# Kernel tuning notes

Measured on AMD Instinct MI355X. Metric: run time of the kernel, lower is better.

## Reference

```python
import jax, jax.numpy as jnp
import numpy as np

N, E, G = 30000, 240000, 1500
EMB, NODE_DIM, EDGE_DIM, TASKS = 300, 9, 3, 12
L_ENC, L_RAT = 5, 2
GAMMA, T_CON = 0.4, 0.2


def _w(key, shape, fan_in):
    return jax.random.normal(key, shape, jnp.float32) / np.float32(np.sqrt(fan_in))


def setup_inputs() -> dict:
    key = jax.random.key(0)
    ks = jax.random.split(key, 32)
    inp = {}
    inp['x'] = jax.random.normal(ks[0], (N, NODE_DIM), jnp.float32)
    inp['edge_attr'] = jax.random.normal(ks[1], (E, EDGE_DIM), jnp.float32)
    inp['edge_index'] = jax.random.randint(ks[2], (2, E), 0, N, jnp.int32)
    b = jnp.sort(jax.random.randint(ks[3], (N,), 0, G, jnp.int32))
    inp['batch'] = b.at[0].set(0).at[-1].set(G - 1)
    u = jax.random.uniform(ks[4], (N, 2), jnp.float32, 1e-6, 1.0 - 1e-6)
    inp['gumbel'] = -jnp.log(-jnp.log(u))  # standard Gumbel noise (tau=1)
    inp['perm'] = jax.random.permutation(ks[5], G).astype(jnp.int32)
    inp['W_enc'] = _w(ks[6], (NODE_DIM, EMB), NODE_DIM)
    inp['b_enc'] = jnp.zeros((EMB,), jnp.float32)
    inp['We_g'] = _w(ks[7], (L_ENC, EDGE_DIM, EMB), EDGE_DIM)
    inp['be_g'] = jnp.zeros((L_ENC, EMB), jnp.float32)
    inp['W1_g'] = _w(ks[8], (L_ENC, EMB, 2 * EMB), EMB)
    inp['b1_g'] = jnp.zeros((L_ENC, 2 * EMB), jnp.float32)
    inp['W2_g'] = _w(ks[9], (L_ENC, 2 * EMB, EMB), 2 * EMB)
    inp['b2_g'] = jnp.zeros((L_ENC, EMB), jnp.float32)
    inp['We_r'] = _w(ks[10], (L_RAT, EDGE_DIM, EMB), EDGE_DIM)
    inp['be_r'] = jnp.zeros((L_RAT, EMB), jnp.float32)
    inp['W1_r'] = _w(ks[11], (L_RAT, EMB, 2 * EMB), EMB)
    inp['b1_r'] = jnp.zeros((L_RAT, 2 * EMB), jnp.float32)
    inp['W2_r'] = _w(ks[12], (L_RAT, 2 * EMB, EMB), 2 * EMB)
    inp['b2_r'] = jnp.zeros((L_RAT, EMB), jnp.float32)
    inp['Wg1'] = _w(ks[13], (EMB, 2 * EMB), EMB)
    inp['bg1'] = jnp.zeros((2 * EMB,), jnp.float32)
    inp['Wg2'] = _w(ks[14], (2 * EMB, 2), 2 * EMB)
    inp['bg2'] = jnp.zeros((2,), jnp.float32)
    inp['Wp1'] = _w(ks[15], (EMB, 2 * EMB), EMB)
    inp['bp1'] = jnp.zeros((2 * EMB,), jnp.float32)
    inp['Wp2'] = _w(ks[16], (2 * EMB, TASKS), 2 * EMB)
    inp['bp2'] = jnp.zeros((TASKS,), jnp.float32)
    return inp


def _gin_stack(x, src, dst, edge_attr, We, be, W1, b1, W2, b2):
    # GIN-style message passing with edge features, residual, JK='last'.
    L = We.shape[0]
    for l in range(L):
        e = edge_attr @ We[l] + be[l]                               # [E, EMB]
        msg = jax.nn.relu(x[src] + e)                                # gather [E, EMB]
        agg = jax.ops.segment_sum(msg, dst, num_segments=x.shape[0])  # scatter [N, EMB]
        h = jax.nn.relu((agg + x) @ W1[l] + b1[l]) @ W2[l] + b2[l]
        if l < L - 1:
            h = jax.nn.relu(h)
        x = x + h  # residual
    return x


def _mlp2(h, Wa, ba, Wb, bb):
    # Linear -> (BN=identity in eval) -> ReLU -> (Dropout=identity) -> Linear
    return jax.nn.relu(h @ Wa + ba) @ Wb + bb


def _forward(x, edge_attr, gumbel, W_enc, b_enc, We_g, be_g, W1_g, b1_g, W2_g, b2_g,
             We_r, be_r, W1_r, b1_r, W2_r, b2_r, Wg1, bg1, Wg2, bg2, Wp1, bp1, Wp2, bp2,
             edge_index, batch, perm):
    src, dst = edge_index[0], edge_index[1]
    cnt = jnp.clip(jax.ops.segment_sum(jnp.ones((x.shape[0],), jnp.float32), batch, num_segments=G), 1.0)[:, None]

    def gmean(v):
        return jax.ops.segment_sum(v, batch, num_segments=G) / cnt

    x_feat = x @ W_enc + b_enc                                      # node encoder
    h_node = _gin_stack(x_feat, src, dst, edge_attr, We_g, be_g, W1_g, b1_g, W2_g, b2_g)
    x_rat = _gin_stack(x_feat, src, dst, edge_attr, We_r, be_r, W1_r, b1_r, W2_r, b2_r)

    gate_logits = _mlp2(x_rat, Wg1, bg1, Wg2, bg2)                  # [N, 2]
    gate = jax.nn.softmax(gate_logits + gumbel, axis=-1)[:, 1:2]     # gumbel-softmax (soft), keep last col

    h_r = gmean(gate * h_node)
    h_env = gmean((1.0 - gate) * h_node)
    r_num = jax.ops.segment_sum(gate, batch, num_segments=G) + 1e-8
    env_num = jax.ops.segment_sum(1.0 - gate, batch, num_segments=G) + 1e-8

    pred_rem = _mlp2(h_r, Wp1, bp1, Wp2, bp2)
    loss_reg = jnp.abs(r_num / (r_num + env_num) - GAMMA).mean()

    h_out = gmean(h_node)
    na = jnp.linalg.norm(h_r, axis=1)
    nb = jnp.linalg.norm(h_out, axis=1)
    nc = jnp.linalg.norm(h_env, axis=1)
    sim = jnp.exp((h_r @ h_out.T) / (na[:, None] * nb[None, :] + 1e-8) / T_CON)
    sim_cp = jnp.exp((h_r @ h_env.T) / (na[:, None] * nc[None, :] + 1e-8) / T_CON)
    pos = jnp.diagonal(sim)
    loss_con = -jnp.log(pos / (sim_cp.sum(axis=1) + pos)).mean()

    pred_rep = _mlp2(h_r + h_env[perm], Wp1, bp1, Wp2, bp2)
    return pred_rep, pred_rem, loss_reg, loss_con


def reference(x, edge_attr, gumbel, W_enc, b_enc, We_g, be_g, W1_g, b1_g, W2_g, b2_g,
              We_r, be_r, W1_r, b1_r, W2_r, b2_r, Wg1, bg1, Wg2, bg2, Wp1, bp1, Wp2, bp2,
              edge_index, batch, perm):
    return _forward(x, edge_attr, gumbel, W_enc, b_enc, We_g, be_g, W1_g, b1_g, W2_g, b2_g,
                    We_r, be_r, W1_r, b1_r, W2_r, b2_r, Wg1, bg1, Wg2, bg2, Wp1, bp1, Wp2, bp2,
                    edge_index, batch, perm)
```

## Files before the change

### kernel.cpp

```cpp
#include <hip/hip_runtime.h>
#include <hip/hip_bf16.h>

typedef __hip_bfloat16 bf16;
typedef __attribute__((ext_vector_type(8))) short bf16x8;
typedef __attribute__((ext_vector_type(4))) float f32x4;

#define NN 30000
#define NE 240000
#define NG 1500
#define EMB 300
#define HID 600
#define NTASK 12
#define SEM 320
#define SHID 608
#define CG 75
#define NBLK_SCAN 118

__device__ __forceinline__ float tof(bf16 v){ return __bfloat162float(v); }
__device__ __forceinline__ bf16  tob(float v){ return __float2bfloat16(v); }
__device__ __forceinline__ float b2f(unsigned short u){ return __uint_as_float(((unsigned)u)<<16); }

__global__ __launch_bounds__(256) void k_zero_i(int* __restrict__ p, int n){
    int i = blockIdx.x*256 + threadIdx.x;
    if (i < n) p[i] = 0;
}

__global__ __launch_bounds__(256) void k_hist(const int* __restrict__ dst, int* __restrict__ deg){
    int e = blockIdx.x*256 + threadIdx.x;
    if (e < NE) atomicAdd(&deg[dst[e]], 1);
}

__global__ __launch_bounds__(256) void k_scanA(const int* __restrict__ deg, int* __restrict__ bsum){
    __shared__ int red[256];
    int b = blockIdx.x, t = threadIdx.x;
    int i = b*256 + t;
    red[t] = (i < NN) ? deg[i] : 0;
    __syncthreads();
    for (int off=128; off>0; off>>=1){ if (t<off) red[t]+=red[t+off]; __syncthreads(); }
    if (t==0) bsum[b] = red[0];
}

__global__ __launch_bounds__(128) void k_scanB(const int* __restrict__ bsum, int* __restrict__ boff){
    __shared__ int s[128];
    int t = threadIdx.x;
    int v = (t < NBLK_SCAN) ? bsum[t] : 0;
    s[t] = v;
    __syncthreads();
    for (int off=1; off<128; off<<=1){
        int add = (t>=off) ? s[t-off] : 0;
        __syncthreads();
        s[t] += add;
        __syncthreads();
    }
    if (t < NBLK_SCAN) boff[t] = s[t] - v;
}

__global__ __launch_bounds__(256) void k_scanC(const int* __restrict__ deg, const int* __restrict__ boff,
                                               int* __restrict__ indptr, int* __restrict__ cursor){
    __shared__ int s[256];
    int b = blockIdx.x, t = threadIdx.x;
    int i = b*256 + t;
    int v = (i < NN) ? deg[i] : 0;
    s[t] = v;
    __syncthreads();
    for (int off=1; off<256; off<<=1){
        int add = (t>=off) ? s[t-off] : 0;
        __syncthreads();
        s[t] += add;
        __syncthreads();
    }
    int excl = s[t] - v + boff[b];
    if (i < NN){ indptr[i] = excl; cursor[i] = excl; }
    if (i == 0) indptr[NN] = NE;
}

__global__ __launch_bounds__(256) void k_scatter(const int* __restrict__ dst, int* __restrict__ cursor,
                                                 int* __restrict__ eid){
    int e = blockIdx.x*256 + threadIdx.x;
    if (e < NE){ int p = atomicAdd(&cursor[dst[e]], 1); eid[p] = e; }
}

__global__ __launch_bounds__(256) void k_eprep(const int* __restrict__ eid, const int* __restrict__ src,
                                               const float* __restrict__ eattr, float4* __restrict__ epack){
    int k = blockIdx.x*256 + threadIdx.x;
    if (k >= NE) return;
    int e = eid[k];
    float4 p;
    p.x = __int_as_float(src[e]);
    p.y = eattr[e*3]; p.z = eattr[e*3+1]; p.w = eattr[e*3+2];
    epack[k] = p;
}

__global__ __launch_bounds__(256) void k_gstart(const int* __restrict__ batch, int* __restrict__ gstart){
    int g = blockIdx.x*256 + threadIdx.x;
    if (g > NG) return;
    if (g == NG){ gstart[NG] = NN; return; }
    int lo=0, hi=NN;
    while (lo<hi){ int mid=(lo+hi)>>1; if (batch[mid] < g) lo=mid+1; else hi=mid; }
    gstart[g] = lo;
}

__global__ __launch_bounds__(256) void k_wprep(const float* __restrict__ W, bf16* __restrict__ Wt,
                                               int K, int Kp, int N){
    __shared__ float t[32][33];
    const float* Wz = W + (size_t)blockIdx.z*K*N;
    bf16* Wtz = Wt + (size_t)blockIdx.z*N*Kp;
    int n0 = blockIdx.x*32, k0 = blockIdx.y*32;
    int tx = threadIdx.x & 31, ty = threadIdx.x >> 5;
    #pragma unroll
    for (int i=0;i<4;i++){
        int k = k0 + ty + i*8, n = n0 + tx;
        t[ty+i*8][tx] = (k<K && n<N) ? Wz[(size_t)k*N+n] : 0.f;
    }
    __syncthreads();
    #pragma unroll
    for (int i=0;i<4;i++){
        int n = n0 + ty + i*8, k = k0 + tx;
        if (n<N && k<Kp) Wtz[(size_t)n*Kp+k] = tob(t[tx][ty+i*8]);
    }
}

__global__ __launch_bounds__(256) void k_encoder(const float* __restrict__ x, const float* __restrict__ W,
                                                 const float* __restrict__ b, bf16* __restrict__ xfeat){
    int idx = blockIdx.x*256 + threadIdx.x;
    if (idx >= NN*EMB) return;
    int n = idx / EMB, c = idx - n*EMB;
    float acc = b[c];
    #pragma unroll
    for (int k=0;k<9;k++) acc += x[n*9+k] * W[k*EMB+c];
    xfeat[(size_t)n*SEM + c] = tob(acc);
}

__global__ __launch_bounds__(256) void k_agg4(const bf16* __restrict__ cur, const float* __restrict__ We,
                      const float* __restrict__ be, const float4* __restrict__ epack,
                      const int* __restrict__ indptr, bf16* __restrict__ apx){
    int idx = blockIdx.x*256 + threadIdx.x;
    if (idx >= NN*CG) return;
    int n = idx / CG, cg = idx - n*CG;
    int c0 = cg*4;
    float w0[4], w1[4], w2[4], bbv[4], acc[4];
    #pragma unroll
    for (int j=0;j<4;j++){
        w0[j] = We[c0+j]; w1[j] = We[EMB+c0+j]; w2[j] = We[2*EMB+c0+j]; bbv[j] = be[c0+j];
    }
    ushort4 hs = *(const ushort4*)&cur[(size_t)n*SEM + c0];
    acc[0]=b2f(hs.x); acc[1]=b2f(hs.y); acc[2]=b2f(hs.z); acc[3]=b2f(hs.w);
    int k  = indptr[n], k1 = indptr[n+1];

    auto accum4 = [&](float4 e0, float4 e1, float4 e2, float4 e3,
                      ushort4 ha, ushort4 hb, ushort4 hc, ushort4 hd){
        float fa[4] = {b2f(ha.x), b2f(ha.y), b2f(ha.z), b2f(ha.w)};
        float fb[4] = {b2f(hb.x), b2f(hb.y), b2f(hb.z), b2f(hb.w)};
        float fc[4] = {b2f(hc.x), b2f(hc.y), b2f(hc.z), b2f(hc.w)};
        float fd[4] = {b2f(hd.x), b2f(hd.y), b2f(hd.z), b2f(hd.w)};
        #pragma unroll
        for (int j=0;j<4;j++){
            float va = fa[j] + e0.y*w0[j] + e0.z*w1[j] + e0.w*w2[j] + bbv[j];
            float vb = fb[j] + e1.y*w0[j] + e1.z*w1[j] + e1.w*w2[j] + bbv[j];
            float vc = fc[j] + e2.y*w0[j] + e2.z*w1[j] + e2.w*w2[j] + bbv[j];
            float vd = fd[j] + e3.y*w0[j] + e3.z*w1[j] + e3.w*w2[j] + bbv[j];
            acc[j] += fmaxf(va, 0.f) + fmaxf(vb, 0.f) + fmaxf(vc, 0.f) + fmaxf(vd, 0.f);
        }
    };

    if (k + 4 <= k1){
        float4 e0 = epack[k], e1 = epack[k+1], e2 = epack[k+2], e3 = epack[k+3];
        ushort4 h0 = *(const ushort4*)&cur[(size_t)__float_as_int(e0.x)*SEM + c0];
        ushort4 h1 = *(const ushort4*)&cur[(size_t)__float_as_int(e1.x)*SEM + c0];
        ushort4 h2 = *(const ushort4*)&cur[(size_t)__float_as_int(e2.x)*SEM + c0];
        ushort4 h3 = *(const ushort4*)&cur[(size_t)__float_as_int(e3.x)*SEM + c0];
        while (k + 8 <= k1){
            float4 f0 = epack[k+4], f1 = epack[k+5], f2 = epack[k+6], f3 = epack[k+7];
            ushort4 g0 = *(const ushort4*)&cur[(size_t)__float_as_int(f0.x)*SEM + c0];
            ushort4 g1 = *(const ushort4*)&cur[(size_t)__float_as_int(f1.x)*SEM + c0];
            ushort4 g2 = *(const ushort4*)&cur[(size_t)__float_as_int(f2.x)*SEM + c0];
            ushort4 g3 = *(const ushort4*)&cur[(size_t)__float_as_int(f3.x)*SEM + c0];
            accum4(e0,e1,e2,e3, h0,h1,h2,h3);
            e0=f0; e1=f1; e2=f2; e3=f3;
            h0=g0; h1=g1; h2=g2; h3=g3;
            k += 4;
        }
        accum4(e0,e1,e2,e3, h0,h1,h2,h3);
        k += 4;
    }
    for (; k < k1; k++){
        float4 e0 = epack[k];
        int s0 = __float_as_int(e0.x);
        ushort4 ha = *(const ushort4*)&cur[(size_t)s0*SEM + c0];
        float fa[4] = {b2f(ha.x), b2f(ha.y), b2f(ha.z), b2f(ha.w)};
        #pragma unroll
        for (int j=0;j<4;j++){
            float va = fa[j] + e0.y*w0[j] + e0.z*w1[j] + e0.w*w2[j] + bbv[j];
            acc[j] += fmaxf(va, 0.f);
        }
    }
    ushort4 o;
    o.x = __bfloat16_as_ushort(tob(acc[0]));
    o.y = __bfloat16_as_ushort(tob(acc[1]));
    o.z = __bfloat16_as_ushort(tob(acc[2]));
    o.w = __bfloat16_as_ushort(tob(acc[3]));
    *(ushort4*)&apx[(size_t)n*SEM + c0] = o;
}

__global__ __launch_bounds__(256) void k_agg4d(const bf16* __restrict__ cur,
                      const float* __restrict__ WeA, const float* __restrict__ beA,
                      const float* __restrict__ WeB, const float* __restrict__ beB,
                      const float4* __restrict__ epack, const int* __restrict__ indptr,
                      bf16* __restrict__ apxA, bf16* __restrict__ apxB){
    int idx = blockIdx.x*256 + threadIdx.x;
    if (idx >= NN*CG) return;
    int n = idx / CG, cg = idx - n*CG;
    int c0 = cg*4;
    float a0[4], a1[4], a2[4], ab[4], accA[4];
    float b0[4], b1[4], b2[4], bb[4], accB[4];
    #pragma unroll
    for (int j=0;j<4;j++){
        a0[j]=WeA[c0+j]; a1[j]=WeA[EMB+c0+j]; a2[j]=WeA[2*EMB+c0+j]; ab[j]=beA[c0+j];
        b0[j]=WeB[c0+j]; b1[j]=WeB[EMB+c0+j]; b2[j]=WeB[2*EMB+c0+j]; bb[j]=beB[c0+j];
    }
    ushort4 hs = *(const ushort4*)&cur[(size_t)n*SEM + c0];
    float fs[4] = {b2f(hs.x), b2f(hs.y), b2f(hs.z), b2f(hs.w)};
    #pragma unroll
    for (int j=0;j<4;j++){ accA[j]=fs[j]; accB[j]=fs[j]; }
    int k = indptr[n], k1 = indptr[n+1];
    for (; k+2 <= k1; k += 2){
        float4 e0 = epack[k], e1 = epack[k+1];
        int s0 = __float_as_int(e0.x), s1 = __float_as_int(e1.x);
        ushort4 ha = *(const ushort4*)&cur[(size_t)s0*SEM + c0];
        ushort4 hb = *(const ushort4*)&cur[(size_t)s1*SEM + c0];
        float fa[4] = {b2f(ha.x), b2f(ha.y), b2f(ha.z), b2f(ha.w)};
        float fb[4] = {b2f(hb.x), b2f(hb.y), b2f(hb.z), b2f(hb.w)};
        #pragma unroll
        for (int j=0;j<4;j++){
            accA[j] += fmaxf(fa[j] + e0.y*a0[j] + e0.z*a1[j] + e0.w*a2[j] + ab[j], 0.f)
                     + fmaxf(fb[j] + e1.y*a0[j] + e1.z*a1[j] + e1.w*a2[j] + ab[j], 0.f);
            accB[j] += fmaxf(fa[j] + e0.y*b0[j] + e0.z*b1[j] + e0.w*b2[j] + bb[j], 0.f)
                     + fmaxf(fb[j] + e1.y*b0[j] + e1.z*b1[j] + e1.w*b2[j] + bb[j], 0.f);
        }
    }
    if (k < k1){
        float4 e0 = epack[k];
        int s0 = __float_as_int(e0.x);
        ushort4 ha = *(const ushort4*)&cur[(size_t)s0*SEM + c0];
        float fa[4] = {b2f(ha.x), b2f(ha.y), b2f(ha.z), b2f(ha.w)};
        #pragma unroll
        for (int j=0;j<4;j++){
            accA[j] += fmaxf(fa[j] + e0.y*a0[j] + e0.z*a1[j] + e0.w*a2[j] + ab[j], 0.f);
            accB[j] += fmaxf(fa[j] + e0.y*b0[j] + e0.z*b1[j] + e0.w*b2[j] + bb[j], 0.f);
        }
    }
    ushort4 oA, oB;
    oA.x=__bfloat16_as_ushort(tob(accA[0])); oA.y=__bfloat16_as_ushort(tob(accA[1]));
    oA.z=__bfloat16_as_ushort(tob(accA[2])); oA.w=__bfloat16_as_ushort(tob(accA[3]));
    oB.x=__bfloat16_as_ushort(tob(accB[0])); oB.y=__bfloat16_as_ushort(tob(accB[1]));
    oB.z=__bfloat16_as_ushort(tob(accB[2])); oB.w=__bfloat16_as_ushort(tob(accB[3]));
    *(ushort4*)&apxA[(size_t)n*SEM + c0] = oA;
    *(ushort4*)&apxB[(size_t)n*SEM + c0] = oB;
}

__global__ __launch_bounds__(256) void k_gemm2(const bf16* __restrict__ A, const bf16* __restrict__ Bt,
        const float* __restrict__ bias, const bf16* __restrict__ R, bf16* __restrict__ C,
        int M, int N, int Kp, int ldc, int relu_out){
    __shared__ __align__(16) char ldsbuf[34816];
    short* lds = reinterpret_cast<short*>(ldsbuf);
    short* Ct  = reinterpret_cast<short*>(ldsbuf);
    const int CS = 136;
    int tid = threadIdx.x;
    int wave = tid >> 6, lane = tid & 63;
    int wm = wave >> 1, wn = wave & 1;
    int m0 = blockIdx.y*128, n0 = blockIdx.x*128;

    int srow = tid >> 1;
    int sq   = (tid & 1) * 2;
    int grA = min(m0 + srow, M-1);
    int grB = min(n0 + srow, N-1);
    const bf16* pA = A  + (size_t)grA*Kp + sq*8;
    const bf16* pB = Bt + (size_t)grB*Kp + sq*8;
    int aoff0 = ((srow>>4)*64 +  sq   *16 + (srow&15))*8;
    int aoff1 = ((srow>>4)*64 + (sq+1)*16 + (srow&15))*8;

    f32x4 acc[4][4];
    #pragma unroll
    for (int i=0;i<4;i++){
        #pragma unroll
        for (int j=0;j<4;j++) acc[i][j] = (f32x4){0.f,0.f,0.f,0.f};
    }

    int KC = Kp >> 5;
    uint4 ra0 = *(const uint4*)(pA);
    uint4 ra1 = *(const uint4*)(pA + 8);
    uint4 rb0 = *(const uint4*)(pB);
    uint4 rb1 = *(const uint4*)(pB + 8);
    *(uint4*)(lds + aoff0)        = ra0;
    *(uint4*)(lds + aoff1)        = ra1;
    *(uint4*)(lds + 4096 + aoff0) = rb0;
    *(uint4*)(lds + 4096 + aoff1) = rb1;
    __syncthreads();
    if (KC > 1){
        ra0 = *(const uint4*)(pA + 32); ra1 = *(const uint4*)(pA + 40);
        rb0 = *(const uint4*)(pB + 32); rb1 = *(const uint4*)(pB + 40);
    }

    for (int kc=0; kc<KC; ++kc){
        short* cbuf = lds + (kc & 1)*8192;
        short* nbuf = lds + ((kc+1) & 1)*8192;
        if (kc+1 < KC){
            *(uint4*)(nbuf + aoff0)        = ra0;
            *(uint4*)(nbuf + aoff1)        = ra1;
            *(uint4*)(nbuf + 4096 + aoff0) = rb0;
            *(uint4*)(nbuf + 4096 + aoff1) = rb1;
            if (kc+2 < KC){
                const bf16* qA = pA + (kc+2)*32;
                const bf16* qB = pB + (kc+2)*32;
                ra0 = *(const uint4*)(qA); ra1 = *(const uint4*)(qA+8);
                rb0 = *(const uint4*)(qB); rb1 = *(const uint4*)(qB+8);
            }
        }
        bf16x8 af[4], bfr[4];
        #pragma unroll
        for (int i=0;i<4;i++) af[i]  = *(const bf16x8*)(cbuf + ((wm*4+i)*64 + lane)*8);
        #pragma unroll
        for (int j=0;j<4;j++) bfr[j] = *(const bf16x8*)(cbuf + 4096 + ((wn*4+j)*64 + lane)*8);
        #pragma unroll
        for (int i=0;i<4;i++){
            #pragma unroll
            for (int j=0;j<4;j++)
                acc[i][j] = __builtin_amdgcn_mfma_f32_16x16x32_bf16(af[i], bfr[j], acc[i][j], 0, 0, 0);
        }
        __syncthreads();
    }

    int lq = lane >> 4, lr = lane & 15;
    #pragma unroll
    for (int i=0;i<4;i++){
        int rl = (wm*4+i)*16 + lq*4;
        #pragma unroll
        for (int j=0;j<4;j++){
            int cl = (wn*4+j)*16 + lr;
            float bv = bias[min(n0+cl, N-1)];
            #pragma unroll
            for (int r=0;r<4;r++){
                float v = acc[i][j][r] + bv;
                if (relu_out) v = fmaxf(v, 0.f);
                Ct[(rl+r)*CS + cl] = (short)__bfloat16_as_ushort(tob(v));
            }
        }
    }
    __syncthreads();
    #pragma unroll
    for (int p=0;p<8;p++){
        int rl = p*16 + (tid>>4);
        int cl = (tid&15)*8;
        int row = m0 + rl, col = n0 + cl;
        if (row < M && col < N){
            union { short s8[8]; uint4 v; } u;
            u.v = *(uint4*)&Ct[rl*CS + cl];
            if (R){
                const bf16* rp = &R[(size_t)row*ldc + col];
                #pragma unroll
                for (int e=0;e<8;e++){
                    float v = b2f((unsigned short)u.s8[e]) + tof(rp[e]);
                    u.s8[e] = (short)__bfloat16_as_ushort(tob(v));
                }
            }
            *(uint4*)&C[(size_t)row*ldc + col] = u.v;
        }
    }
}

__device__ __forceinline__ void stage_tile(const short* __restrict__ P, int RB, int K, int r0, int k0,
                                           short (*lds)[64][8], int tid){
    #pragma unroll
    for (int s=0;s<2;s++){
        int seg = tid*2+s;
        int row = seg>>2, q = seg&3;
        int gr = r0 + row;
        int gk = k0 + q*8;
        union { short s8[8]; uint4 v; } u;
        if (gr < RB && gk + 8 <= K){
            const uint2* p = (const uint2*)(P + (size_t)gr*K + gk);
            uint2 lo = p[0], hi = p[1];
            u.v.x = lo.x; u.v.y = lo.y; u.v.z = hi.x; u.v.w = hi.y;
        } else {
            #pragma unroll
            for (int j=0;j<8;j++){
                int kk = gk + j;
                u.s8[j] = (gr < RB && kk < K) ? P[(size_t)gr*K + kk] : (short)0;
            }
        }
        *(uint4*)&lds[row>>4][q*16 + (row&15)][0] = u.v;
    }
}

__global__ __launch_bounds__(256) void k_sim_mfma(const bf16* __restrict__ A, const bf16* __restrict__ Bt,
                      const float* __restrict__ na, const float* __restrict__ nc, float* __restrict__ C){
    __shared__ __align__(16) short Asl[8][64][8];
    __shared__ __align__(16) short Bsl[8][64][8];
    int tid = threadIdx.x;
    int wave = tid >> 6, lane = tid & 63;
    int wm = wave >> 1, wn = wave & 1;
    int m0 = blockIdx.y*128, n0 = blockIdx.x*128;
    f32x4 acc[4][4];
    #pragma unroll
    for (int i=0;i<4;i++){
        #pragma unroll
        for (int j=0;j<4;j++) acc[i][j] = (f32x4){0.f,0.f,0.f,0.f};
    }
    for (int k0=0; k0<SEM; k0+=32){
        stage_tile((const short*)A,  NG, SEM, m0, k0, Asl, tid);
        stage_tile((const short*)Bt, NG, SEM, n0, k0, Bsl, tid);
        __syncthreads();
        bf16x8 af[4], bfr[4];
        #pragma unroll
        for (int i=0;i<4;i++) af[i]  = *(const bf16x8*)&Asl[wm*4+i][lane][0];
        #pragma unroll
        for (int j=0;j<4;j++) bfr[j] = *(const bf16x8*)&Bsl[wn*4+j][lane][0];
        #pragma unroll
        for (int i=0;i<4;i++){
            #pragma unroll
            for (int j=0;j<4;j++)
                acc[i][j] = __builtin_amdgcn_mfma_f32_16x16x32_bf16(af[i], bfr[j], acc[i][j], 0, 0, 0);
        }
        __syncthreads();
    }
    int lq = lane >> 4, lr = lane & 15;
    #pragma unroll
    for (int i=0;i<4;i++){
        int rb = m0 + (wm*4+i)*16 + lq*4;
        #pragma unroll
        for (int j=0;j<4;j++){
            int col = n0 + (wn*4+j)*16 + lr;
            if (col >= NG) continue;
            float ncj = nc[col];
            #pragma unroll
            for (int r=0;r<4;r++){
                int row = rb + r;
                if (row >= NG) continue;
                C[(size_t)row*NG+col] = expf(acc[i][j][r] * 5.0f / (na[row]*ncj + 1e-8f));
            }
        }
    }
}

__global__ __launch_bounds__(256) void k_gate(const bf16* __restrict__ mid, const float* __restrict__ Wg2,
                      const float* __restrict__ bg2, const float* __restrict__ gumbel, float* __restrict__ gate){
    int gw = blockIdx.x*4 + (threadIdx.x >> 6);
    int lane = threadIdx.x & 63;
    if (gw >= NN) return;
    float s0=0.f, s1=0.f;
    for (int i=lane;i<HID;i+=64){
        float h = tof(mid[(size_t)gw*SHID+i]);
        s0 += h * Wg2[i*2];
        s1 += h * Wg2[i*2+1];
    }
    for (int off=32; off>0; off>>=1){ s0 += __shfl_down(s0, off); s1 += __shfl_down(s1, off); }
    if (lane==0){
        float l0 = s0 + bg2[0] + gumbel[gw*2];
        float l1 = s1 + bg2[1] + gumbel[gw*2+1];
        float m = fmaxf(l0,l1);
        float e0 = expf(l0-m), e1 = expf(l1-m);
        gate[gw] = e1/(e0+e1);
    }
}

__global__ __launch_bounds__(320) void k_pool(const bf16* __restrict__ h, const float* __restrict__ gate,
                      const int* __restrict__ gstart, float* __restrict__ sumh, float* __restrict__ sumgh){
    int g = blockIdx.x, c = threadIdx.x;
    if (c >= EMB) return;
    int n0 = gstart[g], n1 = gstart[g+1];
    float sh=0.f, sg=0.f;
    for (int n=n0;n<n1;n++){
        float v = tof(h[(size_t)n*SEM+c]);
        float gt = gate[n];
        sh += v; sg += gt*v;
    }
    sumh[g*EMB+c] = sh; sumgh[g*EMB+c] = sg;
}

__global__ __launch_bounds__(256) void k_rnum(const float* __restrict__ gate, const int* __restrict__ gstart,
                      float* __restrict__ rnum, float* __restrict__ cntf){
    int g = blockIdx.x*4 + (threadIdx.x >> 6);
    int lane = threadIdx.x & 63;
    if (g >= NG) return;
    int n0 = gstart[g], n1 = gstart[g+1];
    float s=0.f;
    for (int n=n0+lane;n<n1;n+=64) s += gate[n];
    for (int off=32; off>0; off>>=1) s += __shfl_down(s, off);
    if (lane==0){ rnum[g] = s; cntf[g] = (float)(n1-n0); }
}

__global__ __launch_bounds__(256) void k_mean(const float* __restrict__ sumh, const float* __restrict__ sumgh,
                      const float* __restrict__ cntf, float* __restrict__ hr, float* __restrict__ henv,
                      float* __restrict__ hout, bf16* __restrict__ hrb, bf16* __restrict__ henvb){
    int idx = blockIdx.x*256 + threadIdx.x;
    if (idx >= NG*SEM) return;
    int g = idx / SEM, c = idx - g*SEM;
    if (c < EMB){
        int o = g*EMB + c;
        float inv = 1.f / fmaxf(cntf[g], 1.f);
        float sh = sumh[o], sg = sumgh[o];
        float r = sg*inv, e = (sh-sg)*inv;
        hr[o] = r; henv[o] = e; hout[o] = sh*inv;
        hrb[idx] = tob(r); henvb[idx] = tob(e);
    } else {
        hrb[idx] = tob(0.f); henvb[idx] = tob(0.f);
    }
}

__global__ __launch_bounds__(256) void k_pbuild(const float* __restrict__ hr, const float* __restrict__ henv,
                      const int* __restrict__ perm, bf16* __restrict__ P){
    int idx = blockIdx.x*256 + threadIdx.x;
    if (idx >= NG*SEM) return;
    int g = idx / SEM, c = idx - g*SEM;
    if (c < EMB){
        float v = hr[g*EMB+c];
        P[idx] = tob(v);
        P[(size_t)(NG+g)*SEM + c] = tob(v + henv[(size_t)perm[g]*EMB + c]);
    } else {
        P[idx] = tob(0.f);
        P[(size_t)(NG+g)*SEM + c] = tob(0.f);
    }
}

__global__ __launch_bounds__(256) void k_norm(const float* __restrict__ hr, const float* __restrict__ henv,
                      const float* __restrict__ hout, float* __restrict__ na, float* __restrict__ nc,
                      float* __restrict__ pos){
    int g = blockIdx.x*4 + (threadIdx.x >> 6);
    int lane = threadIdx.x & 63;
    if (g >= NG) return;
    float srr=0.f, soo=0.f, see=0.f, sro=0.f;
    for (int c=lane;c<EMB;c+=64){
        float r=hr[g*EMB+c], o=hout[g*EMB+c], e=henv[g*EMB+c];
        srr += r*r; soo += o*o; see += e*e; sro += r*o;
    }
    for (int off=32; off>0; off>>=1){
        srr += __shfl_down(srr,off); soo += __shfl_down(soo,off);
        see += __shfl_down(see,off); sro += __shfl_down(sro,off);
    }
    if (lane==0){
        float a = sqrtf(srr), b = sqrtf(soo), c2 = sqrtf(see);
        na[g] = a; nc[g] = c2;
        pos[g] = expf(sro/(a*b + 1e-8f) * 5.0f);
    }
}

__global__ __launch_bounds__(256) void k_rowsum(const float* __restrict__ simcp, float* __restrict__ S){
    __shared__ float red[256];
    int g = blockIdx.x, t = threadIdx.x;
    float s = 0.f;
    for (int j=t;j<NG;j+=256) s += simcp[(size_t)g*NG+j];
    red[t]=s; __syncthreads();
    for (int off=128; off>0; off>>=1){ if (t<off) red[t]+=red[t+off]; __syncthreads(); }
    if (t==0) S[g]=red[0];
}

__global__ __launch_bounds__(256) void k_pred(const bf16* __restrict__ hidP, const float* __restrict__ Wp2,
                      const float* __restrict__ bp2, float* __restrict__ out){
    int r = blockIdx.x*4 + (threadIdx.x >> 6);
    int lane = threadIdx.x & 63;
    if (r >= 2*NG) return;
    float acc[NTASK];
    #pragma unroll
    for (int t=0;t<NTASK;t++) acc[t] = 0.f;
    for (int i=lane;i<HID;i+=64){
        float h = tof(hidP[(size_t)r*SHID+i]);
        const float4* wp = (const float4*)&Wp2[i*NTASK];
        float4 wa = wp[0], wb = wp[1], wc = wp[2];
        acc[0]+=h*wa.x; acc[1]+=h*wa.y; acc[2]+=h*wa.z; acc[3]+=h*wa.w;
        acc[4]+=h*wb.x; acc[5]+=h*wb.y; acc[6]+=h*wb.z; acc[7]+=h*wb.w;
        acc[8]+=h*wc.x; acc[9]+=h*wc.y; acc[10]+=h*wc.z; acc[11]+=h*wc.w;
    }
    #pragma unroll
    for (int t=0;t<NTASK;t++){
        for (int off=32; off>0; off>>=1) acc[t] += __shfl_down(acc[t], off);
    }
    if (lane==0){
        float* dst = (r < NG) ? &out[NG*NTASK + r*NTASK] : &out[(r-NG)*NTASK];
        #pragma unroll
        for (int t=0;t<NTASK;t++) dst[t] = acc[t] + bp2[t];
    }
}

__global__ __launch_bounds__(256) void k_loss(const float* __restrict__ cntf, const float* __restrict__ rnum,
                      const float* __restrict__ pos, const float* __restrict__ S, float* __restrict__ out){
    __shared__ float ra[256], rb[256];
    int t = threadIdx.x;
    float a=0.f, b=0.f;
    for (int g=t; g<NG; g+=256){
        float r = rnum[g] + 1e-8f;
        float e = (cntf[g] - rnum[g]) + 1e-8f;
        a += fabsf(r/(r+e) - 0.4f);
        float p = pos[g];
        b += -logf(p/(S[g]+p));
    }
    ra[t]=a; rb[t]=b; __syncthreads();
    for (int off=128; off>0; off>>=1){ if (t<off){ ra[t]+=ra[t+off]; rb[t]+=rb[t+off]; } __syncthreads(); }
    if (t==0){
        out[2*NG*NTASK]   = ra[0]/NG;
        out[2*NG*NTASK+1] = rb[0]/NG;
    }
}

extern "C" void kernel_launch(void* const* d_in, const int* in_sizes, int n_in,
                              void* d_out, int out_size, void* d_ws, size_t ws_size,
                              hipStream_t stream) {
    const float* x      = (const float*)d_in[0];
    const float* eattr  = (const float*)d_in[1];
    const int*   eidx   = (const int*)d_in[2];
    const int*   batch  = (const int*)d_in[3];
    const float* gumbel = (const float*)d_in[4];
    const int*   perm   = (const int*)d_in[5];
    const float* W_enc  = (const float*)d_in[6];
    const float* b_enc  = (const float*)d_in[7];
    const float* We_g   = (const float*)d_in[8];
    const float* be_g   = (const float*)d_in[9];
    const float* W1_g   = (const float*)d_in[10];
    const float* b1_g   = (const float*)d_in[11];
    const float* W2_g   = (const float*)d_in[12];
    const float* b2_g   = (const float*)d_in[13];
    const float* We_r   = (const float*)d_in[14];
    const float* be_r   = (const float*)d_in[15];
    const float* W1_r   = (const float*)d_in[16];
    const float* b1_r   = (const float*)d_in[17];
    const float* W2_r   = (const float*)d_in[18];
    const float* b2_r   = (const float*)d_in[19];
    const float* Wg1    = (const float*)d_in[20];
    const float* bg1    = (const float*)d_in[21];
    const float* Wg2    = (const float*)d_in[22];
    const float* bg2    = (const float*)d_in[23];
    const float* Wp1    = (const float*)d_in[24];
    const float* bp1    = (const float*)d_in[25];
    const float* Wp2    = (const float*)d_in[26];
    const float* bp2    = (const float*)d_in[27];
    float* out = (float*)d_out;

    const int* srcArr = eidx;
    const int* dstArr = eidx + NE;

    char* w = (char*)d_ws;
    size_t off = 0;
    auto alloc = [&](size_t bytes)->char*{ char* p = w + off; off += (bytes + 255) & ~(size_t)255; return p; };
    bf16* xfeat = (bf16*)alloc((size_t)NN*SEM*2);
    bf16* cur   = (bf16*)alloc((size_t)NN*SEM*2);
    bf16* apx   = (bf16*)alloc((size_t)NN*SEM*2);
    bf16* apx2  = (bf16*)alloc((size_t)NN*SEM*2);
    char* midc  = alloc((size_t)NN*SHID*2);
    bf16* mid   = (bf16*)midc;
    float* simcp = (float*)midc;
    bf16* Pbuf   = (bf16*)(midc + 12*1024*1024);
    bf16* hidP   = (bf16*)(midc + 20*1024*1024);
    bf16* wt1g  = (bf16*)alloc((size_t)5*HID*SEM*2);
    bf16* wt2g  = (bf16*)alloc((size_t)5*EMB*SHID*2);
    bf16* wt1r  = (bf16*)alloc((size_t)2*HID*SEM*2);
    bf16* wt2r  = (bf16*)alloc((size_t)2*EMB*SHID*2);
    bf16* wtg1  = (bf16*)alloc((size_t)HID*SEM*2);
    bf16* wtp1  = (bf16*)alloc((size_t)HID*SEM*2);
    float4* epack = (float4*)alloc((size_t)NE*16);
    float* gate  = (float*)alloc((size_t)NN*4);
    float* sumh  = (float*)alloc((size_t)NG*EMB*4);
    float* sumgh = (float*)alloc((size_t)NG*EMB*4);
    float* hr    = (float*)alloc((size_t)NG*EMB*4);
    float* henv  = (float*)alloc((size_t)NG*EMB*4);
    float* hout  = (float*)alloc((size_t)NG*EMB*4);
    bf16* hrb    = (bf16*)alloc((size_t)NG*SEM*2);
    bf16* henvb  = (bf16*)alloc((size_t)NG*SEM*2);
    float* rnum  = (float*)alloc(NG*4);
    float* cntf  = (float*)alloc(NG*4);
    float* na    = (float*)alloc(NG*4);
    float* ncv   = (float*)alloc(NG*4);
    float* pos   = (float*)alloc(NG*4);
    float* Ssum  = (float*)alloc(NG*4);
    int* deg     = (int*)alloc((size_t)NN*4);
    int* indptr  = (int*)alloc((size_t)(NN+1)*4);
    int* cursor  = (int*)alloc((size_t)NN*4);
    int* eid     = (int*)alloc((size_t)NE*4);
    int* gstart  = (int*)alloc((size_t)(NG+1)*4);
    int* bsum    = (int*)alloc((size_t)NBLK_SCAN*4);
    int* boff    = (int*)alloc((size_t)NBLK_SCAN*4);

    const int NB_NE  = (NE+255)/256;
    const int NB_NC  = (NN*EMB+255)/256;
    const int NB_AG  = (NN*CG+255)/256;
    const int NB_GP  = (NG*SEM+255)/256;

    k_zero_i <<<(NN+255)/256, 256, 0, stream>>>(deg, NN);
    k_hist   <<<NB_NE, 256, 0, stream>>>(dstArr, deg);
    k_scanA  <<<NBLK_SCAN, 256, 0, stream>>>(deg, bsum);
    k_scanB  <<<1, 128, 0, stream>>>(bsum, boff);
    k_scanC  <<<NBLK_SCAN, 256, 0, stream>>>(deg, boff, indptr, cursor);
    k_scatter<<<NB_NE, 256, 0, stream>>>(dstArr, cursor, eid);
    k_eprep  <<<NB_NE, 256, 0, stream>>>(eid, srcArr, eattr, epack);
    k_gstart <<<(NG+256)/256, 256, 0, stream>>>(batch, gstart);

    {
        dim3 g1t((HID+31)/32, SEM/32, 5);
        dim3 g2t((EMB+31)/32, SHID/32, 5);
        k_wprep<<<g1t, 256, 0, stream>>>(W1_g, wt1g, EMB, SEM, HID);
        k_wprep<<<g2t, 256, 0, stream>>>(W2_g, wt2g, HID, SHID, EMB);
        dim3 g1t2((HID+31)/32, SEM/32, 2);
        dim3 g2t2((EMB+31)/32, SHID/32, 2);
        k_wprep<<<g1t2, 256, 0, stream>>>(W1_r, wt1r, EMB, SEM, HID);
        k_wprep<<<g2t2, 256, 0, stream>>>(W2_r, wt2r, HID, SHID, EMB);
        dim3 g1t1((HID+31)/32, SEM/32, 1);
        k_wprep<<<g1t1, 256, 0, stream>>>(Wg1, wtg1, EMB, SEM, HID);
        k_wprep<<<g1t1, 256, 0, stream>>>(Wp1, wtp1, EMB, SEM, HID);
    }

    dim3 gm1((HID+127)/128, (NN+127)/128);
    dim3 gm2((EMB+127)/128, (NN+127)/128);

    k_encoder<<<NB_NC, 256, 0, stream>>>(x, W_enc, b_enc, xfeat);

    k_agg4d<<<NB_AG, 256, 0, stream>>>(xfeat, We_r, be_r, We_g, be_g, epack, indptr, apx, apx2);

    for (int l=0; l<2; l++){
        const bf16* in = (l==0) ? xfeat : cur;
        if (l > 0)
            k_agg4 <<<NB_AG, 256, 0, stream>>>(in, We_r + l*3*EMB, be_r + l*EMB, epack, indptr, apx);
        k_gemm2<<<gm1, 256, 0, stream>>>(apx, wt1r + (size_t)l*HID*SEM, b1_r + l*HID, nullptr, mid,
                                         NN, HID, SEM, SHID, 1);
        k_gemm2<<<gm2, 256, 0, stream>>>(mid, wt2r + (size_t)l*EMB*SHID, b2_r + l*EMB, in, cur,
                                         NN, EMB, SHID, SEM, (l<1)?1:0);
    }
    k_gemm2<<<gm1, 256, 0, stream>>>(cur, wtg1, bg1, nullptr, mid, NN, HID, SEM, SHID, 1);
    k_gate<<<NN/4, 256, 0, stream>>>(mid, Wg2, bg2, gumbel, gate);

    for (int l=0; l<5; l++){
        const bf16* in = (l==0) ? xfeat : cur;
        const bf16* ap = (l==0) ? apx2 : apx;
        if (l > 0)
            k_agg4 <<<NB_AG, 256, 0, stream>>>(in, We_g + l*3*EMB, be_g + l*EMB, epack, indptr, apx);
        k_gemm2<<<gm1, 256, 0, stream>>>(ap, wt1g + (size_t)l*HID*SEM, b1_g + l*HID, nullptr, mid,
                                         NN, HID, SEM, SHID, 1);
        k_gemm2<<<gm2, 256, 0, stream>>>(mid, wt2g + (size_t)l*EMB*SHID, b2_g + l*EMB, in, cur,
                                         NN, EMB, SHID, SEM, (l<4)?1:0);
    }

    k_pool  <<<NG, 320, 0, stream>>>(cur, gate, gstart, sumh, sumgh);
    k_rnum  <<<(NG+3)/4, 256, 0, stream>>>(gate, gstart, rnum, cntf);
    k_mean  <<<NB_GP, 256, 0, stream>>>(sumh, sumgh, cntf, hr, henv, hout, hrb, henvb);
    k_pbuild<<<NB_GP, 256, 0, stream>>>(hr, henv, perm, Pbuf);
    k_norm  <<<(NG+3)/4, 256, 0, stream>>>(hr, henv, hout, na, ncv, pos);
    dim3 gsim((NG+127)/128, (NG+127)/128);
    k_sim_mfma<<<gsim, 256, 0, stream>>>(hrb, henvb, na, ncv, simcp);
    k_rowsum<<<NG, 256, 0, stream>>>(simcp, Ssum);
    dim3 gph((HID+127)/128, (2*NG+127)/128);
    k_gemm2<<<gph, 256, 0, stream>>>(Pbuf, wtp1, bp1, nullptr, hidP, 2*NG, HID, SEM, SHID, 1);
    k_pred  <<<(2*NG+3)/4, 256, 0, stream>>>(hidP, Wp2, bp2, out);
    k_loss  <<<1, 256, 0, stream>>>(cntf, rnum, pos, Ssum, out);
}
```

Before: 997.4 us.

## Batch independent rationale and graph GIN layers into paired z-dimension launches

The rationale encoder (2 layers) and the first layers of the graph encoder are independent. They are now interleaved and run as combined launches, with blockIdx.z choosing the stack, through new k_agg4z and k_gemm2z wrappers around shared device bodies. The goal is fewer kernel launches and fewer serialized small-grid tail phases, so the GPU gets more concurrent work. It costs separate cur and mid buffers per stack, which raises the memory footprint, and the schedule in the host code becomes harder to follow.

Result: no change. 986.1 us (-1.1%).

```diff
diff --git a/kernel.cpp b/kernel.cpp
--- a/kernel.cpp
+++ b/kernel.cpp
@@ -131,11 +131,9 @@
     xfeat[(size_t)n*SEM + c] = tob(acc);
 }
 
-__global__ __launch_bounds__(256) void k_agg4(const bf16* __restrict__ cur, const float* __restrict__ We,
+__device__ __forceinline__ void agg4_body(const bf16* __restrict__ cur, const float* __restrict__ We,
                       const float* __restrict__ be, const float4* __restrict__ epack,
-                      const int* __restrict__ indptr, bf16* __restrict__ apx){
-    int idx = blockIdx.x*256 + threadIdx.x;
-    if (idx >= NN*CG) return;
+                      const int* __restrict__ indptr, bf16* __restrict__ apx, int idx){
     int n = idx / CG, cg = idx - n*CG;
     int c0 = cg*4;
     float w0[4], w1[4], w2[4], bbv[4], acc[4];
@@ -202,6 +200,25 @@
     *(ushort4*)&apx[(size_t)n*SEM + c0] = o;
 }
 
+__global__ __launch_bounds__(256) void k_agg4(const bf16* __restrict__ cur, const float* __restrict__ We,
+                      const float* __restrict__ be, const float4* __restrict__ epack,
+                      const int* __restrict__ indptr, bf16* __restrict__ apx){
+    int idx = blockIdx.x*256 + threadIdx.x;
+    if (idx >= NN*CG) return;
+    agg4_body(cur, We, be, epack, indptr, apx, idx);
+}
+
+__global__ __launch_bounds__(256) void k_agg4z(const bf16* __restrict__ cur0, const bf16* __restrict__ cur1,
+                      const float* __restrict__ We0, const float* __restrict__ We1,
+                      const float* __restrict__ be0, const float* __restrict__ be1,
+                      const float4* __restrict__ epack, const int* __restrict__ indptr,
+                      bf16* __restrict__ apx0, bf16* __restrict__ apx1){
+    int idx = blockIdx.x*256 + threadIdx.x;
+    if (idx >= NN*CG) return;
+    if (blockIdx.z == 0) agg4_body(cur0, We0, be0, epack, indptr, apx0, idx);
+    else                 agg4_body(cur1, We1, be1, epack, indptr, apx1, idx);
+}
+
 __global__ __launch_bounds__(256) void k_agg4d(const bf16* __restrict__ cur,
                       const float* __restrict__ WeA, const float* __restrict__ beA,
                       const float* __restrict__ WeB, const float* __restrict__ beB,
@@ -258,12 +275,10 @@
     *(ushort4*)&apxB[(size_t)n*SEM + c0] = oB;
 }
 
-__global__ __launch_bounds__(256) void k_gemm2(const bf16* __restrict__ A, const bf16* __restrict__ Bt,
+__device__ __forceinline__ void gemm_body(const bf16* __restrict__ A, const bf16* __restrict__ Bt,
         const float* __restrict__ bias, const bf16* __restrict__ R, bf16* __restrict__ C,
-        int M, int N, int Kp, int ldc, int relu_out){
-    __shared__ __align__(16) char ldsbuf[34816];
-    short* lds = reinterpret_cast<short*>(ldsbuf);
-    short* Ct  = reinterpret_cast<short*>(ldsbuf);
+        int M, int N, int Kp, int ldc, int relu_out, short* lds){
+    short* Ct = lds;
     const int CS = 136;
     int tid = threadIdx.x;
     int wave = tid >> 6, lane = tid & 63;
@@ -366,6 +381,25 @@
             *(uint4*)&C[(size_t)row*ldc + col] = u.v;
         }
     }
+}
+
+__global__ __launch_bounds__(256) void k_gemm2(const bf16* __restrict__ A, const bf16* __restrict__ Bt,
+        const float* __restrict__ bias, const bf16* __restrict__ R, bf16* __restrict__ C,
+        int M, int N, int Kp, int ldc, int relu_out){
+    __shared__ __align__(16) char ldsbuf[34816];
+    gemm_body(A, Bt, bias, R, C, M, N, Kp, ldc, relu_out, (short*)ldsbuf);
+}
+
+__global__ __launch_bounds__(256) void k_gemm2z(
+        const bf16* __restrict__ A0, const bf16* __restrict__ A1,
+        const bf16* __restrict__ Bt0, const bf16* __restrict__ Bt1,
+        const float* __restrict__ bias0, const float* __restrict__ bias1,
+        const bf16* __restrict__ R0, const bf16* __restrict__ R1,
+        bf16* __restrict__ C0, bf16* __restrict__ C1,
+        int M, int N, int Kp, int ldc, int relu0, int relu1){
+    __shared__ __align__(16) char ldsbuf[34816];
+    if (blockIdx.z == 0) gemm_body(A0, Bt0, bias0, R0, C0, M, N, Kp, ldc, relu0, (short*)ldsbuf);
+    else                 gemm_body(A1, Bt1, bias1, R1, C1, M, N, Kp, ldc, relu1, (short*)ldsbuf);
 }
 
 __device__ __forceinline__ void stage_tile(const short* __restrict__ P, int RB, int K, int r0, int k0,
@@ -641,14 +675,16 @@
     size_t off = 0;
     auto alloc = [&](size_t bytes)->char*{ char* p = w + off; off += (bytes + 255) & ~(size_t)255; return p; };
     bf16* xfeat = (bf16*)alloc((size_t)NN*SEM*2);
-    bf16* cur   = (bf16*)alloc((size_t)NN*SEM*2);
+    bf16* cur_r = (bf16*)alloc((size_t)NN*SEM*2);
+    bf16* cur_g = (bf16*)alloc((size_t)NN*SEM*2);
     bf16* apx   = (bf16*)alloc((size_t)NN*SEM*2);
     bf16* apx2  = (bf16*)alloc((size_t)NN*SEM*2);
     char* midc  = alloc((size_t)NN*SHID*2);
-    bf16* mid   = (bf16*)midc;
+    bf16* mid_r = (bf16*)midc;
     float* simcp = (float*)midc;
     bf16* Pbuf   = (bf16*)(midc + 12*1024*1024);
     bf16* hidP   = (bf16*)(midc + 20*1024*1024);
+    bf16* mid_g = (bf16*)alloc((size_t)NN*SHID*2);
     bf16* wt1g  = (bf16*)alloc((size_t)5*HID*SEM*2);
     bf16* wt2g  = (bf16*)alloc((size_t)5*EMB*SHID*2);
     bf16* wt1r  = (bf16*)alloc((size_t)2*HID*SEM*2);
@@ -706,37 +742,46 @@
         k_wprep<<<g1t1, 256, 0, stream>>>(Wp1, wtp1, EMB, SEM, HID);
     }
 
+    dim3 gm1z((HID+127)/128, (NN+127)/128, 2);
+    dim3 gm2z((EMB+127)/128, (NN+127)/128, 2);
     dim3 gm1((HID+127)/128, (NN+127)/128);
     dim3 gm2((EMB+127)/128, (NN+127)/128);
+    dim3 gagz(NB_AG, 1, 2);
 
     k_encoder<<<NB_NC, 256, 0, stream>>>(x, W_enc, b_enc, xfeat);
 
     k_agg4d<<<NB_AG, 256, 0, stream>>>(xfeat, We_r, be_r, We_g, be_g, epack, indptr, apx, apx2);
-
-    for (int l=0; l<2; l++){
-        const bf16* in = (l==0) ? xfeat : cur;
-        if (l > 0)
-            k_agg4 <<<NB_AG, 256, 0, stream>>>(in, We_r + l*3*EMB, be_r + l*EMB, epack, indptr, apx);
-        k_gemm2<<<gm1, 256, 0, stream>>>(apx, wt1r + (size_t)l*HID*SEM, b1_r + l*HID, nullptr, mid,
+    k_gemm2z<<<gm1z, 256, 0, stream>>>(apx, apx2, wt1r, wt1g, b1_r, b1_g,
+                                       nullptr, nullptr, mid_r, mid_g, NN, HID, SEM, SHID, 1, 1);
+    k_gemm2z<<<gm2z, 256, 0, stream>>>(mid_r, mid_g, wt2r, wt2g, b2_r, b2_g,
+                                       xfeat, xfeat, cur_r, cur_g, NN, EMB, SHID, SEM, 1, 1);
+
+    k_agg4z<<<gagz, 256, 0, stream>>>(cur_r, cur_g, We_r + 3*EMB, We_g + 3*EMB, be_r + EMB, be_g + EMB,
+                                      epack, indptr, apx, apx2);
+    k_gemm2z<<<gm1z, 256, 0, stream>>>(apx, apx2, wt1r + (size_t)HID*SEM, wt1g + (size_t)HID*SEM,
+                                       b1_r + HID, b1_g + HID, nullptr, nullptr, mid_r, mid_g,
+                                       NN, HID, SEM, SHID, 1, 1);
+    k_gemm2z<<<gm2z, 256, 0, stream>>>(mid_r, mid_g, wt2r + (size_t)EMB*SHID, wt2g + (size_t)EMB*SHID,
+                                       b2_r + EMB, b2_g + EMB, cur_r, cur_g, cur_r, cur_g,
+                                       NN, EMB, SHID, SEM, 0, 1);
+
+    k_agg4 <<<NB_AG, 256, 0, stream>>>(cur_g, We_g + 2*3*EMB, be_g + 2*EMB, epack, indptr, apx2);
+    k_gemm2z<<<gm1z, 256, 0, stream>>>(cur_r, apx2, wtg1, wt1g + (size_t)2*HID*SEM,
+                                       bg1, b1_g + 2*HID, nullptr, nullptr, mid_r, mid_g,
+                                       NN, HID, SEM, SHID, 1, 1);
+    k_gemm2<<<gm2, 256, 0, stream>>>(mid_g, wt2g + (size_t)2*EMB*SHID, b2_g + 2*EMB, cur_g, cur_g,
+                                     NN, EMB, SHID, SEM, 1);
+    k_gate<<<NN/4, 256, 0, stream>>>(mid_r, Wg2, bg2, gumbel, gate);
+
+    for (int l=3; l<5; l++){
+        k_agg4 <<<NB_AG, 256, 0, stream>>>(cur_g, We_g + l*3*EMB, be_g + l*EMB, epack, indptr, apx2);
+        k_gemm2<<<gm1, 256, 0, stream>>>(apx2, wt1g + (size_t)l*HID*SEM, b1_g + l*HID, nullptr, mid_g,
                                          NN, HID, SEM, SHID, 1);
-        k_gemm2<<<gm2, 256, 0, stream>>>(mid, wt2r + (size_t)l*EMB*SHID, b2_r + l*EMB, in, cur,
-                                         NN, EMB, SHID, SEM, (l<1)?1:0);
-    }
-    k_gemm2<<<gm1, 256, 0, stream>>>(cur, wtg1, bg1, nullptr, mid, NN, HID, SEM, SHID, 1);
-    k_gate<<<NN/4, 256, 0, stream>>>(mid, Wg2, bg2, gumbel, gate);
-
-    for (int l=0; l<5; l++){
-        const bf16* in = (l==0) ? xfeat : cur;
-        const bf16* ap = (l==0) ? apx2 : apx;
-        if (l > 0)
-            k_agg4 <<<NB_AG, 256, 0, stream>>>(in, We_g + l*3*EMB, be_g + l*EMB, epack, indptr, apx);
-        k_gemm2<<<gm1, 256, 0, stream>>>(ap, wt1g + (size_t)l*HID*SEM, b1_g + l*HID, nullptr, mid,
-                                         NN, HID, SEM, SHID, 1);
-        k_gemm2<<<gm2, 256, 0, stream>>>(mid, wt2g + (size_t)l*EMB*SHID, b2_g + l*EMB, in, cur,
+        k_gemm2<<<gm2, 256, 0, stream>>>(mid_g, wt2g + (size_t)l*EMB*SHID, b2_g + l*EMB, cur_g, cur_g,
                                          NN, EMB, SHID, SEM, (l<4)?1:0);
     }
 
-    k_pool  <<<NG, 320, 0, stream>>>(cur, gate, gstart, sumh, sumgh);
+    k_pool  <<<NG, 320, 0, stream>>>(cur_g, gate, gstart, sumh, sumgh);
     k_rnum  <<<(NG+3)/4, 256, 0, stream>>>(gate, gstart, rnum, cntf);
     k_mean  <<<NB_GP, 256, 0, stream>>>(sumh, sumgh, cntf, hr, henv, hout, hrb, henvb);
     k_pbuild<<<NB_GP, 256, 0, stream>>>(hr, henv, perm, Pbuf);
```
